# Optimization experiments

Measured on AMD Instinct MI355X. Metric: run time of the kernel, lower is better.

## Reference

```python
import jax, jax.numpy as jnp
import numpy as np

N = 50000        # nodes
E = 800000       # edges (avg degree 16)
OBS = 128        # observation_dim
HID = 64         # hidden_dim (per head)
H1 = 4           # heads in conv1
ACT = 32         # action_dim
NEG_SLOPE = 0.2  # GATv2 default negative_slope


def setup_inputs() -> dict:
    key = jax.random.key(0)
    ks = jax.random.split(key, 10)
    s = 0.05
    x = jax.random.normal(ks[0], (N, OBS), jnp.float32)
    edge_index = jax.random.randint(ks[1], (2, E), 0, N, dtype=jnp.int32)
    # conv1: GATv2Conv(OBS -> HID, heads=4, concat=True)
    W1l = jax.random.normal(ks[2], (OBS, H1 * HID), jnp.float32) * s  # lin_l (source)
    W1r = jax.random.normal(ks[3], (OBS, H1 * HID), jnp.float32) * s  # lin_r (target)
    att1 = jax.random.normal(ks[4], (H1, HID), jnp.float32) * s
    b1 = jnp.zeros((H1 * HID,), jnp.float32)
    # conv2: GATv2Conv(H1*HID -> ACT, heads=1, concat=False)
    W2l = jax.random.normal(ks[5], (H1 * HID, ACT), jnp.float32) * s
    W2r = jax.random.normal(ks[6], (H1 * HID, ACT), jnp.float32) * s
    att2 = jax.random.normal(ks[7], (1, ACT), jnp.float32) * s
    b2 = jnp.zeros((ACT,), jnp.float32)
    return {"x": x, "edge_index": edge_index, "W1l": W1l, "W1r": W1r,
            "att1": att1, "b1": b1, "W2l": W2l, "W2r": W2r,
            "att2": att2, "b2": b2}


def gatv2_layer(x, Wl, Wr, att, bias, src, dst, heads, out_ch, concat):
    """PyG GATv2Conv (add_self_loops=False, share_weights=False)."""
    n = x.shape[0]
    xl = (x @ Wl).reshape(n, heads, out_ch)  # source transform
    xr = (x @ Wr).reshape(n, heads, out_ch)  # target transform
    e = xl[src] + xr[dst]                    # [E, H, C] gathered messages
    g = jnp.where(e > 0, e, NEG_SLOPE * e)   # LeakyReLU
    logits = jnp.einsum('ehc,hc->eh', g, att)  # [E, H]
    # segment softmax over incoming edges of each destination node
    m = jax.ops.segment_max(logits, dst, num_segments=n)      # [N, H]
    ex = jnp.exp(logits - m[dst])
    denom = jax.ops.segment_sum(ex, dst, num_segments=n)      # [N, H]
    alpha = ex / denom[dst]                                   # [E, H]
    out = jax.ops.segment_sum(xl[src] * alpha[:, :, None], dst, num_segments=n)
    out = out.reshape(n, heads * out_ch) if concat else out.mean(axis=1)
    return out + bias


def reference(x, edge_index, W1l, W1r, att1, b1, W2l, W2r, att2, b2):
    src, dst = edge_index[0], edge_index[1]
    h = jax.nn.relu(gatv2_layer(x, W1l, W1r, att1, b1, src, dst, H1, HID, True))
    out = gatv2_layer(h, W2l, W2r, att2, b2, src, dst, 1, ACT, False)
    return out
```

## Files before the change

kernel.cpp:

```cpp
#include <hip/hip_runtime.h>
#include <hip/hip_bf16.h>
#include <math.h>


#define OBS 128
#define HID 64
#define H1 4
#define C1 256
#define ACT 32
#define PAD 128
#define NEG_SLOPE 0.2f
#define LOG2E 1.4426950408889634f

typedef __attribute__((ext_vector_type(2))) _Float16 h2;
typedef __attribute__((ext_vector_type(8))) _Float16 half8;
typedef __attribute__((ext_vector_type(4))) float f32x4;

__device__ inline h2 bc_h2(unsigned u) { return __builtin_bit_cast(h2, u); }
__device__ inline unsigned bc_u(h2 v) { return __builtin_bit_cast(unsigned, v); }
__device__ inline h2 lrelu2(h2 e) {
  const h2 k = {(_Float16)NEG_SLOPE, (_Float16)NEG_SLOPE};
  return __builtin_elementwise_max(e, e * k);
}

__global__ void prep(const float* __restrict__ W1l, const float* __restrict__ W1r,
                     const float* __restrict__ W2l, const float* __restrict__ W2r,
                     _Float16* __restrict__ W1t, _Float16* __restrict__ W2t,
                     const int* __restrict__ src, const int* __restrict__ dst,
                     int* __restrict__ cursor, int* __restrict__ esrc_p,
                     int E, int csrBlocks) {
  int b = blockIdx.x;
  if (b < csrBlocks) {
    int e = b * 256 + threadIdx.x;
    if (e < E) {
      int d = dst[e];
      int slot = atomicAdd(&cursor[d], 1);
      if (slot < PAD) esrc_p[((size_t)d << 7) + slot] = src[e];
    }
    return;
  }
  int i = (b - csrBlocks) * 256 + threadIdx.x;
  if (i < 512 * 128) {
    int n = i >> 7, k = i & 127;
    float v = (n < C1) ? W1l[k * C1 + n] : W1r[k * C1 + (n - C1)];
    W1t[i] = (_Float16)v;
  }
  int j = i - 512 * 128;
  if (j >= 0 && j < 64 * 256) {
    int n = j >> 8, c = j & 255;
    float v = (n < ACT) ? W2l[c * ACT + n] : W2r[c * ACT + (n - ACT)];
    W2t[j] = (_Float16)v;
  }
}

__global__ __launch_bounds__(256) void gemm_mfma1(
    const float* __restrict__ xf,
    const _Float16* __restrict__ W1t,
    _Float16* __restrict__ XLh,
    _Float16* __restrict__ XRh,
    int M) {
  const int LDK = 136;
  __shared__ _Float16 As[128 * 136];
  __shared__ _Float16 Bs[128 * 136];
  const int tid = threadIdx.x;
  const int lane = tid & 63;
  const int wid = tid >> 6;
  const int wm = (wid & 1) * 64, wn = (wid >> 1) * 64;
  const int rowBase = blockIdx.x * 128;
  const int l15 = lane & 15, lq = lane >> 4;

#pragma unroll
  for (int cc = 0; cc < 8; ++cc) {
    int q = cc * 256 + tid;
    int r = q >> 4;
    int kc = (q & 15) * 8;
    int grow = rowBase + r;
    float4 f0 = make_float4(0.f, 0.f, 0.f, 0.f), f1 = f0;
    if (grow < M) {
      f0 = *(const float4*)(xf + (size_t)grow * 128 + kc);
      f1 = *(const float4*)(xf + (size_t)grow * 128 + kc + 4);
    }
    h2 p0 = {(_Float16)f0.x, (_Float16)f0.y};
    h2 p1 = {(_Float16)f0.z, (_Float16)f0.w};
    h2 p2 = {(_Float16)f1.x, (_Float16)f1.y};
    h2 p3 = {(_Float16)f1.z, (_Float16)f1.w};
    *(int4*)(As + r * LDK + kc) = make_int4(bc_u(p0), bc_u(p1), bc_u(p2), bc_u(p3));
  }
#pragma unroll
  for (int cc = 0; cc < 8; ++cc) {
    int q = cc * 256 + tid;
    int r = q >> 4;
    int kc = (q & 15) * 8;
    *(int4*)(Bs + r * LDK + kc) = *(const int4*)(W1t + (size_t)r * 128 + kc);
  }
  __syncthreads();

  for (int cb = 0; cb < 4; ++cb) {
    f32x4 acc[4][4];
#pragma unroll
    for (int i = 0; i < 4; ++i)
#pragma unroll
      for (int j = 0; j < 4; ++j) acc[i][j] = (f32x4){0.f, 0.f, 0.f, 0.f};

#pragma unroll
    for (int ks = 0; ks < 4; ++ks) {
      half8 af[4], bf[4];
#pragma unroll
      for (int t = 0; t < 4; ++t) {
        af[t] = *(const half8*)(As + (wm + t * 16 + l15) * LDK + ks * 32 + lq * 8);
        bf[t] = *(const half8*)(Bs + (wn + t * 16 + l15) * LDK + ks * 32 + lq * 8);
      }
#pragma unroll
      for (int mt = 0; mt < 4; ++mt)
#pragma unroll
        for (int nt = 0; nt < 4; ++nt)
          acc[mt][nt] = __builtin_amdgcn_mfma_f32_16x16x32_f16(
              af[mt], bf[nt], acc[mt][nt], 0, 0, 0);
    }

    _Float16* outp = (cb < 2) ? XLh : XRh;
    int colBase = (cb & 1) * 128;
#pragma unroll
    for (int mt = 0; mt < 4; ++mt) {
#pragma unroll
      for (int r = 0; r < 4; ++r) {
        int row = rowBase + wm + mt * 16 + lq * 4 + r;
        if (row >= M) continue;
#pragma unroll
        for (int nt = 0; nt < 4; ++nt) {
          int col = colBase + wn + nt * 16 + l15;
          outp[(size_t)row * C1 + col] = (_Float16)acc[mt][nt][r];
        }
      }
    }

    if (cb < 3) {
      __syncthreads();
#pragma unroll
      for (int cc = 0; cc < 8; ++cc) {
        int q = cc * 256 + tid;
        int r = q >> 4;
        int kc = (q & 15) * 8;
        *(int4*)(Bs + r * LDK + kc) =
            *(const int4*)(W1t + (size_t)((cb + 1) * 128 + r) * 128 + kc);
      }
      __syncthreads();
    }
  }
}

__global__ __launch_bounds__(256) void gemm_mfma2(
    const _Float16* __restrict__ Hh,
    const _Float16* __restrict__ W2t,
    _Float16* __restrict__ H2h,
    int M) {
  const int LDK = 136;
  __shared__ _Float16 As[128 * 136];
  __shared__ _Float16 Bs[64 * 136];
  const int tid = threadIdx.x;
  const int lane = tid & 63;
  const int wid = tid >> 6;
  const int wm = (wid & 1) * 64, wn = (wid >> 1) * 32;
  const int rowBase = blockIdx.x * 128;

  f32x4 acc[4][2];
#pragma unroll
  for (int i = 0; i < 4; ++i)
#pragma unroll
    for (int j = 0; j < 2; ++j) acc[i][j] = (f32x4){0.f, 0.f, 0.f, 0.f};

  const int l15 = lane & 15, lq = lane >> 4;

  for (int kb = 0; kb < 256; kb += 128) {
#pragma unroll
    for (int cc = 0; cc < 8; ++cc) {
      int q = cc * 256 + tid;
      int r = q >> 4;
      int kc = (q & 15) * 8;
      int grow = rowBase + r;
      int4 av = make_int4(0, 0, 0, 0);
      if (grow < M) av = *(const int4*)(Hh + (size_t)grow * 256 + kb + kc);
      *(int4*)(As + r * LDK + kc) = av;
    }
#pragma unroll
    for (int cc = 0; cc < 4; ++cc) {
      int q = cc * 256 + tid;
      int r = q >> 4;
      int kc = (q & 15) * 8;
      *(int4*)(Bs + r * LDK + kc) = *(const int4*)(W2t + (size_t)r * 256 + kb + kc);
    }
    __syncthreads();

#pragma unroll
    for (int ks = 0; ks < 4; ++ks) {
      half8 af[4], bf[2];
#pragma unroll
      for (int t = 0; t < 4; ++t)
        af[t] = *(const half8*)(As + (wm + t * 16 + l15) * LDK + ks * 32 + lq * 8);
#pragma unroll
      for (int t = 0; t < 2; ++t)
        bf[t] = *(const half8*)(Bs + (wn + t * 16 + l15) * LDK + ks * 32 + lq * 8);
#pragma unroll
      for (int mt = 0; mt < 4; ++mt)
#pragma unroll
        for (int nt = 0; nt < 2; ++nt)
          acc[mt][nt] = __builtin_amdgcn_mfma_f32_16x16x32_f16(
              af[mt], bf[nt], acc[mt][nt], 0, 0, 0);
    }
    __syncthreads();
  }

#pragma unroll
  for (int mt = 0; mt < 4; ++mt) {
#pragma unroll
    for (int r = 0; r < 4; ++r) {
      int row = rowBase + wm + mt * 16 + lq * 4 + r;
      if (row >= M) continue;
#pragma unroll
      for (int nt = 0; nt < 2; ++nt) {
        int col = wn + nt * 16 + l15;
        H2h[(size_t)row * 64 + col] = (_Float16)acc[mt][nt][r];
      }
    }
  }
}

__global__ __launch_bounds__(256) void agg1(const _Float16* __restrict__ XLh,
                                            const _Float16* XRh,
                                            const float* __restrict__ att1,
                                            const float* __restrict__ b1,
                                            const int* __restrict__ degp,
                                            const int* __restrict__ esrc_p,
                                            _Float16* Hh, int n_nodes) {
  int wave = threadIdx.x >> 6;
  int lane = threadIdx.x & 63;
  int n = blockIdx.x * 4 + wave;
  if (n >= n_nodes) return;
  int sl = lane & 31;
  int half = lane >> 5;
  int c8 = sl * 8;

  const char* XLb = (const char*)XLh + c8 * 2;
  int4 xru = *(const int4*)((const char*)XRh + (n << 9) + c8 * 2);
  h2 xr[4] = {bc_h2(xru.x), bc_h2(xru.y), bc_h2(xru.z), bc_h2(xru.w)};
  const float* ap = att1 + (c8 >> 6) * HID + (c8 & 63);
  float4 a0 = *(const float4*)ap;
  float4 a1 = *(const float4*)(ap + 4);
  h2 av[4] = {{(_Float16)(a0.x * LOG2E), (_Float16)(a0.y * LOG2E)},
              {(_Float16)(a0.z * LOG2E), (_Float16)(a0.w * LOG2E)},
              {(_Float16)(a1.x * LOG2E), (_Float16)(a1.y * LOG2E)},
              {(_Float16)(a1.z * LOG2E), (_Float16)(a1.w * LOG2E)}};

  int d = min(degp[n], PAD);
  const int* ep = esrc_p + ((size_t)n << 7);
  float l = 0.f;
  h2 acc[4];
#pragma unroll
  for (int k = 0; k < 4; ++k) acc[k] = (h2){(_Float16)0.f, (_Float16)0.f};

  int base = 0;
  int dmain = d & ~7;
  for (; base < dmain; base += 8) {
    int s0 = ep[base + half];
    int s1 = ep[base + 2 + half];
    int s2 = ep[base + 4 + half];
    int s3 = ep[base + 6 + half];
    int4 u0 = *(const int4*)(XLb + (s0 << 9));
    int4 u1 = *(const int4*)(XLb + (s1 << 9));
    int4 u2 = *(const int4*)(XLb + (s2 << 9));
    int4 u3 = *(const int4*)(XLb + (s3 << 9));
    h2 x0[4] = {bc_h2(u0.x), bc_h2(u0.y), bc_h2(u0.z), bc_h2(u0.w)};
    h2 x1[4] = {bc_h2(u1.x), bc_h2(u1.y), bc_h2(u1.z), bc_h2(u1.w)};
    h2 x2[4] = {bc_h2(u2.x), bc_h2(u2.y), bc_h2(u2.z), bc_h2(u2.w)};
    h2 x3[4] = {bc_h2(u3.x), bc_h2(u3.y), bc_h2(u3.z), bc_h2(u3.w)};
    float c0 = 0.f, c1 = 0.f, c2 = 0.f, c3 = 0.f;
#pragma unroll
    for (int k = 0; k < 4; ++k) {
      c0 = __builtin_amdgcn_fdot2(lrelu2(x0[k] + xr[k]), av[k], c0, false);
      c1 = __builtin_amdgcn_fdot2(lrelu2(x1[k] + xr[k]), av[k], c1, false);
      c2 = __builtin_amdgcn_fdot2(lrelu2(x2[k] + xr[k]), av[k], c2, false);
      c3 = __builtin_amdgcn_fdot2(lrelu2(x3[k] + xr[k]), av[k], c3, false);
    }
    c0 += __shfl_xor(c0, 1); c1 += __shfl_xor(c1, 1);
    c2 += __shfl_xor(c2, 1); c3 += __shfl_xor(c3, 1);
    c0 += __shfl_xor(c0, 2); c1 += __shfl_xor(c1, 2);
    c2 += __shfl_xor(c2, 2); c3 += __shfl_xor(c3, 2);
    c0 += __shfl_xor(c0, 4); c1 += __shfl_xor(c1, 4);
    c2 += __shfl_xor(c2, 4); c3 += __shfl_xor(c3, 4);
    float p0 = __builtin_amdgcn_exp2f(c0);
    float p1 = __builtin_amdgcn_exp2f(c1);
    float p2 = __builtin_amdgcn_exp2f(c2);
    float p3 = __builtin_amdgcn_exp2f(c3);
    l += (p0 + p1) + (p2 + p3);
    _Float16 q0 = (_Float16)p0, q1 = (_Float16)p1, q2 = (_Float16)p2, q3 = (_Float16)p3;
    h2 w0 = {q0, q0}, w1 = {q1, q1}, w2 = {q2, q2}, w3 = {q3, q3};
#pragma unroll
    for (int k = 0; k < 4; ++k)
      acc[k] = acc[k] + w0 * x0[k] + w1 * x1[k] + w2 * x2[k] + w3 * x3[k];
  }
  if (base + 4 <= d) {
    int s0 = ep[base + half];
    int s1 = ep[base + 2 + half];
    int4 u0 = *(const int4*)(XLb + (s0 << 9));
    int4 u1 = *(const int4*)(XLb + (s1 << 9));
    h2 x0[4] = {bc_h2(u0.x), bc_h2(u0.y), bc_h2(u0.z), bc_h2(u0.w)};
    h2 x1[4] = {bc_h2(u1.x), bc_h2(u1.y), bc_h2(u1.z), bc_h2(u1.w)};
    float c0 = 0.f, c1 = 0.f;
#pragma unroll
    for (int k = 0; k < 4; ++k) {
      c0 = __builtin_amdgcn_fdot2(lrelu2(x0[k] + xr[k]), av[k], c0, false);
      c1 = __builtin_amdgcn_fdot2(lrelu2(x1[k] + xr[k]), av[k], c1, false);
    }
    c0 += __shfl_xor(c0, 1); c1 += __shfl_xor(c1, 1);
    c0 += __shfl_xor(c0, 2); c1 += __shfl_xor(c1, 2);
    c0 += __shfl_xor(c0, 4); c1 += __shfl_xor(c1, 4);
    float p0 = __builtin_amdgcn_exp2f(c0);
    float p1 = __builtin_amdgcn_exp2f(c1);
    l += p0 + p1;
    _Float16 q0 = (_Float16)p0, q1 = (_Float16)p1;
    h2 w0 = {q0, q0}, w1 = {q1, q1};
#pragma unroll
    for (int k = 0; k < 4; ++k) acc[k] = acc[k] + w0 * x0[k] + w1 * x1[k];
    base += 4;
  }
  if (base < d) {
    int e0 = base + half, e1 = base + 2 + half;
    bool v0 = e0 < d, v1 = e1 < d;
    int s0 = ep[v0 ? e0 : 0];
    int s1 = ep[v1 ? e1 : 0];
    int4 u0 = *(const int4*)(XLb + (s0 << 9));
    int4 u1 = *(const int4*)(XLb + (s1 << 9));
    h2 x0[4] = {bc_h2(u0.x), bc_h2(u0.y), bc_h2(u0.z), bc_h2(u0.w)};
    h2 x1[4] = {bc_h2(u1.x), bc_h2(u1.y), bc_h2(u1.z), bc_h2(u1.w)};
    float c0 = 0.f, c1 = 0.f;
#pragma unroll
    for (int k = 0; k < 4; ++k) {
      c0 = __builtin_amdgcn_fdot2(lrelu2(x0[k] + xr[k]), av[k], c0, false);
      c1 = __builtin_amdgcn_fdot2(lrelu2(x1[k] + xr[k]), av[k], c1, false);
    }
    c0 += __shfl_xor(c0, 1); c1 += __shfl_xor(c1, 1);
    c0 += __shfl_xor(c0, 2); c1 += __shfl_xor(c1, 2);
    c0 += __shfl_xor(c0, 4); c1 += __shfl_xor(c1, 4);
    float p0 = v0 ? __builtin_amdgcn_exp2f(c0) : 0.f;
    float p1 = v1 ? __builtin_amdgcn_exp2f(c1) : 0.f;
    l += p0 + p1;
    _Float16 q0 = (_Float16)p0, q1 = (_Float16)p1;
    h2 w0 = {q0, q0}, w1 = {q1, q1};
#pragma unroll
    for (int k = 0; k < 4; ++k) acc[k] = acc[k] + w0 * x0[k] + w1 * x1[k];
  }

  l += __shfl_xor(l, 32);
#pragma unroll
  for (int k = 0; k < 4; ++k) {
    unsigned o = __shfl_xor((int)bc_u(acc[k]), 32);
    acc[k] = acc[k] + bc_h2(o);
  }

  float inv = (d > 0) ? 1.f / l : 0.f;
  if (half == 0) {
    float4 b0 = *(const float4*)(b1 + c8);
    float4 b3 = *(const float4*)(b1 + c8 + 4);
    float o0 = fmaxf((float)acc[0][0] * inv + b0.x, 0.f);
    float o1 = fmaxf((float)acc[0][1] * inv + b0.y, 0.f);
    float o2 = fmaxf((float)acc[1][0] * inv + b0.z, 0.f);
    float o3 = fmaxf((float)acc[1][1] * inv + b0.w, 0.f);
    float o4 = fmaxf((float)acc[2][0] * inv + b3.x, 0.f);
    float o5 = fmaxf((float)acc[2][1] * inv + b3.y, 0.f);
    float o6 = fmaxf((float)acc[3][0] * inv + b3.z, 0.f);
    float o7 = fmaxf((float)acc[3][1] * inv + b3.w, 0.f);
    h2 q0 = {(_Float16)o0, (_Float16)o1};
    h2 q1 = {(_Float16)o2, (_Float16)o3};
    h2 q2 = {(_Float16)o4, (_Float16)o5};
    h2 q3 = {(_Float16)o6, (_Float16)o7};
    *(int4*)((char*)Hh + (n << 9) + c8 * 2) =
        make_int4(bc_u(q0), bc_u(q1), bc_u(q2), bc_u(q3));
  }
}

__global__ __launch_bounds__(256) void agg2(const _Float16* __restrict__ H2h,
                                            const float* __restrict__ att2,
                                            const float* __restrict__ b2,
                                            const int* __restrict__ degp,
                                            const int* __restrict__ esrc_p,
                                            float* __restrict__ out, int n_nodes) {
  int wave = threadIdx.x >> 6;
  int lane = threadIdx.x & 63;
  int n = blockIdx.x * 4 + wave;
  if (n >= n_nodes) return;
  int g = lane >> 3;
  int j = lane & 7;
  int c4 = j * 4;

  const char* Hb = (const char*)H2h + c4 * 2;
  uint2 hru = *(const uint2*)((const char*)H2h + (n << 7) + 64 + c4 * 2);
  h2 hr0 = bc_h2(hru.x), hr1 = bc_h2(hru.y);
  float4 af = *(const float4*)(att2 + c4);
  h2 a0 = {(_Float16)(af.x * LOG2E), (_Float16)(af.y * LOG2E)};
  h2 a1 = {(_Float16)(af.z * LOG2E), (_Float16)(af.w * LOG2E)};

  int d = min(degp[n], PAD);
  const int* ep = esrc_p + ((size_t)n << 7);
  float l = 0.f;
  h2 acc0 = {(_Float16)0.f, (_Float16)0.f}, acc1 = acc0;

  int base = 0;
  int dmain = d & ~7;
  for (; base < dmain; base += 8) {
    int s = ep[base + g];
    uint2 u = *(const uint2*)(Hb + (s << 7));
    h2 h0 = bc_h2(u.x), h1 = bc_h2(u.y);
    float c = __builtin_amdgcn_fdot2(lrelu2(h0 + hr0), a0,
              __builtin_amdgcn_fdot2(lrelu2(h1 + hr1), a1, 0.f, false), false);
    c += __shfl_xor(c, 1);
    c += __shfl_xor(c, 2);
    c += __shfl_xor(c, 4);
    float p = __builtin_amdgcn_exp2f(c);
    l += p;
    _Float16 ph = (_Float16)p;
    h2 p2 = {ph, ph};
    acc0 = acc0 + p2 * h0;
    acc1 = acc1 + p2 * h1;
  }
  if (base < d) {
    int e = base + g;
    bool v = e < d;
    int s = ep[v ? e : 0];
    uint2 u = *(const uint2*)(Hb + (s << 7));
    h2 h0 = bc_h2(u.x), h1 = bc_h2(u.y);
    float c = __builtin_amdgcn_fdot2(lrelu2(h0 + hr0), a0,
              __builtin_amdgcn_fdot2(lrelu2(h1 + hr1), a1, 0.f, false), false);
    c += __shfl_xor(c, 1);
    c += __shfl_xor(c, 2);
    c += __shfl_xor(c, 4);
    float p = v ? __builtin_amdgcn_exp2f(c) : 0.f;
    l += p;
    _Float16 ph = (_Float16)p;
    h2 p2 = {ph, ph};
    acc0 = acc0 + p2 * h0;
    acc1 = acc1 + p2 * h1;
  }

#pragma unroll
  for (int o = 8; o < 64; o <<= 1) {
    l += __shfl_xor(l, o);
    acc0 = acc0 + bc_h2((unsigned)__shfl_xor((int)bc_u(acc0), o));
    acc1 = acc1 + bc_h2((unsigned)__shfl_xor((int)bc_u(acc1), o));
  }

  float inv = (d > 0) ? 1.f / l : 0.f;
  if (g == 0) {
    float4 bb = *(const float4*)(b2 + c4);
    float4 o;
    o.x = (float)acc0[0] * inv + bb.x;
    o.y = (float)acc0[1] * inv + bb.y;
    o.z = (float)acc1[0] * inv + bb.z;
    o.w = (float)acc1[1] * inv + bb.w;
    *(float4*)(out + (size_t)n * ACT + c4) = o;
  }
}

extern "C" void kernel_launch(void* const* d_in, const int* in_sizes, int n_in,
                              void* d_out, int out_size, void* d_ws, size_t ws_size,
                              hipStream_t stream) {
  (void)n_in; (void)out_size; (void)ws_size;
  const float* x    = (const float*)d_in[0];
  const int*   ei   = (const int*)d_in[1];
  const float* W1l  = (const float*)d_in[2];
  const float* W1r  = (const float*)d_in[3];
  const float* att1 = (const float*)d_in[4];
  const float* b1   = (const float*)d_in[5];
  const float* W2l  = (const float*)d_in[6];
  const float* W2r  = (const float*)d_in[7];
  const float* att2 = (const float*)d_in[8];
  const float* b2   = (const float*)d_in[9];
  float* out = (float*)d_out;

  const int N = in_sizes[0] / OBS;
  const int E = in_sizes[1] / 2;
  const int* src = ei;
  const int* dst = ei + E;

  _Float16* XLh = (_Float16*)d_ws;
  _Float16* XRh = XLh + (size_t)N * C1;
  _Float16* W1t = XRh + (size_t)N * C1;
  _Float16* W2t = W1t + 512 * 128;
  int* cursor   = (int*)(W2t + 64 * 256);
  int* esrc_p   = cursor + N;
  _Float16* Hh  = XRh;
  _Float16* H2h = XLh;

  (void)hipMemsetAsync(cursor, 0, sizeof(int) * (size_t)N, stream);

  dim3 b256(256);
  int csrBlocks = (E + 255) / 256;
  int packBlocks = (512 * 128 + 64 * 256 + 255) / 256;
  int gr128 = (N + 127) / 128;

  prep<<<csrBlocks + packBlocks, b256, 0, stream>>>(
      W1l, W1r, W2l, W2r, W1t, W2t, src, dst, cursor, esrc_p, E, csrBlocks);
  gemm_mfma1<<<gr128, b256, 0, stream>>>(x, W1t, XLh, XRh, N);
  agg1<<<(N + 3) / 4, b256, 0, stream>>>(XLh, XRh, att1, b1, cursor, esrc_p, Hh, N);
  gemm_mfma2<<<gr128, b256, 0, stream>>>(Hh, W2t, H2h, N);
  agg2<<<(N + 3) / 4, b256, 0, stream>>>(H2h, att2, b2, cursor, esrc_p, out, N);
}
```

Before: 246.4 us.

## Fuse CSR build into GEMM1, shrink edge indices to u16, split agg1 by head

Cursor zeroing moves into the weight-pack kernel, which removes the memset, and the CSR scatter now runs as extra blocks of the first GEMM launch so the two overlap. Source indices in the padded adjacency are stored as 16-bit values, halving index traffic. That only holds while N stays below 65536. agg1 now gives each head its own grid-y slice, with 8 lanes covering one head's 64 channels and 8 edges processed per step. This raises parallelism but re-reads degree and index data once per head. The CSR blocks inherit the GEMM kernel's large shared-memory footprint, which may limit their occupancy.

```diff
diff --git a/kernel.cpp b/kernel.cpp
--- a/kernel.cpp
+++ b/kernel.cpp
@@ -23,23 +23,12 @@
   return __builtin_elementwise_max(e, e * k);
 }
 
-__global__ void prep(const float* __restrict__ W1l, const float* __restrict__ W1r,
-                     const float* __restrict__ W2l, const float* __restrict__ W2r,
-                     _Float16* __restrict__ W1t, _Float16* __restrict__ W2t,
-                     const int* __restrict__ src, const int* __restrict__ dst,
-                     int* __restrict__ cursor, int* __restrict__ esrc_p,
-                     int E, int csrBlocks) {
-  int b = blockIdx.x;
-  if (b < csrBlocks) {
-    int e = b * 256 + threadIdx.x;
-    if (e < E) {
-      int d = dst[e];
-      int slot = atomicAdd(&cursor[d], 1);
-      if (slot < PAD) esrc_p[((size_t)d << 7) + slot] = src[e];
-    }
-    return;
-  }
-  int i = (b - csrBlocks) * 256 + threadIdx.x;
+__global__ void prep0(const float* __restrict__ W1l, const float* __restrict__ W1r,
+                      const float* __restrict__ W2l, const float* __restrict__ W2r,
+                      _Float16* __restrict__ W1t, _Float16* __restrict__ W2t,
+                      int* __restrict__ cursor, int N) {
+  int i = blockIdx.x * 256 + threadIdx.x;
+  if (i < N) cursor[i] = 0;
   if (i < 512 * 128) {
     int n = i >> 7, k = i & 127;
     float v = (n < C1) ? W1l[k * C1 + n] : W1r[k * C1 + (n - C1)];
@@ -53,15 +42,29 @@
   }
 }
 
-__global__ __launch_bounds__(256) void gemm_mfma1(
+__global__ __launch_bounds__(256) void gemm1_csr(
     const float* __restrict__ xf,
     const _Float16* __restrict__ W1t,
     _Float16* __restrict__ XLh,
     _Float16* __restrict__ XRh,
-    int M) {
+    int M,
+    const int* __restrict__ src, const int* __restrict__ dst,
+    int* __restrict__ cursor, unsigned short* __restrict__ esrc_p,
+    int E, int gemmBlocks) {
   const int LDK = 136;
   __shared__ _Float16 As[128 * 136];
   __shared__ _Float16 Bs[128 * 136];
+
+  if ((int)blockIdx.x >= gemmBlocks) {
+    int e = ((int)blockIdx.x - gemmBlocks) * 256 + threadIdx.x;
+    if (e < E) {
+      int d = dst[e];
+      int slot = atomicAdd(&cursor[d], 1);
+      if (slot < PAD) esrc_p[((size_t)d << 7) + slot] = (unsigned short)src[e];
+    }
+    return;
+  }
+
   const int tid = threadIdx.x;
   const int lane = tid & 63;
   const int wid = tid >> 6;
@@ -230,20 +233,21 @@
                                             const float* __restrict__ att1,
                                             const float* __restrict__ b1,
                                             const int* __restrict__ degp,
-                                            const int* __restrict__ esrc_p,
+                                            const unsigned short* __restrict__ esrc_p,
                                             _Float16* Hh, int n_nodes) {
   int wave = threadIdx.x >> 6;
   int lane = threadIdx.x & 63;
   int n = blockIdx.x * 4 + wave;
+  int head = blockIdx.y;
   if (n >= n_nodes) return;
-  int sl = lane & 31;
-  int half = lane >> 5;
-  int c8 = sl * 8;
-
-  const char* XLb = (const char*)XLh + c8 * 2;
-  int4 xru = *(const int4*)((const char*)XRh + (n << 9) + c8 * 2);
+  int g = lane >> 3;
+  int j = lane & 7;
+  int co = head * 128 + j * 16;
+
+  const char* XLb = (const char*)XLh + co;
+  int4 xru = *(const int4*)((const char*)XRh + ((size_t)n << 9) + co);
   h2 xr[4] = {bc_h2(xru.x), bc_h2(xru.y), bc_h2(xru.z), bc_h2(xru.w)};
-  const float* ap = att1 + (c8 >> 6) * HID + (c8 & 63);
+  const float* ap = att1 + head * HID + j * 8;
   float4 a0 = *(const float4*)ap;
   float4 a1 = *(const float4*)(ap + 4);
   h2 av[4] = {{(_Float16)(a0.x * LOG2E), (_Float16)(a0.y * LOG2E)},
@@ -252,57 +256,19 @@
               {(_Float16)(a1.z * LOG2E), (_Float16)(a1.w * LOG2E)}};
 
   int d = min(degp[n], PAD);
-  const int* ep = esrc_p + ((size_t)n << 7);
+  const unsigned short* ep = esrc_p + ((size_t)n << 7);
   float l = 0.f;
   h2 acc[4];
 #pragma unroll
   for (int k = 0; k < 4; ++k) acc[k] = (h2){(_Float16)0.f, (_Float16)0.f};
 
   int base = 0;
-  int dmain = d & ~7;
-  for (; base < dmain; base += 8) {
-    int s0 = ep[base + half];
-    int s1 = ep[base + 2 + half];
-    int s2 = ep[base + 4 + half];
-    int s3 = ep[base + 6 + half];
-    int4 u0 = *(const int4*)(XLb + (s0 << 9));
-    int4 u1 = *(const int4*)(XLb + (s1 << 9));
-    int4 u2 = *(const int4*)(XLb + (s2 << 9));
-    int4 u3 = *(const int4*)(XLb + (s3 << 9));
-    h2 x0[4] = {bc_h2(u0.x), bc_h2(u0.y), bc_h2(u0.z), bc_h2(u0.w)};
-    h2 x1[4] = {bc_h2(u1.x), bc_h2(u1.y), bc_h2(u1.z), bc_h2(u1.w)};
-    h2 x2[4] = {bc_h2(u2.x), bc_h2(u2.y), bc_h2(u2.z), bc_h2(u2.w)};
-    h2 x3[4] = {bc_h2(u3.x), bc_h2(u3.y), bc_h2(u3.z), bc_h2(u3.w)};
-    float c0 = 0.f, c1 = 0.f, c2 = 0.f, c3 = 0.f;
-#pragma unroll
-    for (int k = 0; k < 4; ++k) {
-      c0 = __builtin_amdgcn_fdot2(lrelu2(x0[k] + xr[k]), av[k], c0, false);
-      c1 = __builtin_amdgcn_fdot2(lrelu2(x1[k] + xr[k]), av[k], c1, false);
-      c2 = __builtin_amdgcn_fdot2(lrelu2(x2[k] + xr[k]), av[k], c2, false);
-      c3 = __builtin_amdgcn_fdot2(lrelu2(x3[k] + xr[k]), av[k], c3, false);
-    }
-    c0 += __shfl_xor(c0, 1); c1 += __shfl_xor(c1, 1);
-    c2 += __shfl_xor(c2, 1); c3 += __shfl_xor(c3, 1);
-    c0 += __shfl_xor(c0, 2); c1 += __shfl_xor(c1, 2);
-    c2 += __shfl_xor(c2, 2); c3 += __shfl_xor(c3, 2);
-    c0 += __shfl_xor(c0, 4); c1 += __shfl_xor(c1, 4);
-    c2 += __shfl_xor(c2, 4); c3 += __shfl_xor(c3, 4);
-    float p0 = __builtin_amdgcn_exp2f(c0);
-    float p1 = __builtin_amdgcn_exp2f(c1);
-    float p2 = __builtin_amdgcn_exp2f(c2);
-    float p3 = __builtin_amdgcn_exp2f(c3);
-    l += (p0 + p1) + (p2 + p3);
-    _Float16 q0 = (_Float16)p0, q1 = (_Float16)p1, q2 = (_Float16)p2, q3 = (_Float16)p3;
-    h2 w0 = {q0, q0}, w1 = {q1, q1}, w2 = {q2, q2}, w3 = {q3, q3};
-#pragma unroll
-    for (int k = 0; k < 4; ++k)
-      acc[k] = acc[k] + w0 * x0[k] + w1 * x1[k] + w2 * x2[k] + w3 * x3[k];
-  }
-  if (base + 4 <= d) {
-    int s0 = ep[base + half];
-    int s1 = ep[base + 2 + half];
-    int4 u0 = *(const int4*)(XLb + (s0 << 9));
-    int4 u1 = *(const int4*)(XLb + (s1 << 9));
+  int dmain = d & ~15;
+  for (; base < dmain; base += 16) {
+    int s0 = ep[base + g];
+    int s1 = ep[base + 8 + g];
+    int4 u0 = *(const int4*)(XLb + ((size_t)s0 << 9));
+    int4 u1 = *(const int4*)(XLb + ((size_t)s1 << 9));
     h2 x0[4] = {bc_h2(u0.x), bc_h2(u0.y), bc_h2(u0.z), bc_h2(u0.w)};
     h2 x1[4] = {bc_h2(u1.x), bc_h2(u1.y), bc_h2(u1.z), bc_h2(u1.w)};
     float c0 = 0.f, c1 = 0.f;
@@ -321,46 +287,60 @@
     h2 w0 = {q0, q0}, w1 = {q1, q1};
 #pragma unroll
     for (int k = 0; k < 4; ++k) acc[k] = acc[k] + w0 * x0[k] + w1 * x1[k];
-    base += 4;
+  }
+  if (base + 8 <= d) {
+    int s0 = ep[base + g];
+    int4 u0 = *(const int4*)(XLb + ((size_t)s0 << 9));
+    h2 x0[4] = {bc_h2(u0.x), bc_h2(u0.y), bc_h2(u0.z), bc_h2(u0.w)};
+    float c0 = 0.f;
+#pragma unroll
+    for (int k = 0; k < 4; ++k)
+      c0 = __builtin_amdgcn_fdot2(lrelu2(x0[k] + xr[k]), av[k], c0, false);
+    c0 += __shfl_xor(c0, 1);
+    c0 += __shfl_xor(c0, 2);
+    c0 += __shfl_xor(c0, 4);
+    float p0 = __builtin_amdgcn_exp2f(c0);
+    l += p0;
+    _Float16 q0 = (_Float16)p0;
+    h2 w0 = {q0, q0};
+#pragma unroll
+    for (int k = 0; k < 4; ++k) acc[k] = acc[k] + w0 * x0[k];
+    base += 8;
   }
   if (base < d) {
-    int e0 = base + half, e1 = base + 2 + half;
-    bool v0 = e0 < d, v1 = e1 < d;
-    int s0 = ep[v0 ? e0 : 0];
-    int s1 = ep[v1 ? e1 : 0];
-    int4 u0 = *(const int4*)(XLb + (s0 << 9));
-    int4 u1 = *(const int4*)(XLb + (s1 << 9));
+    int e = base + g;
+    bool v = e < d;
+    int s0 = ep[v ? e : 0];
+    int4 u0 = *(const int4*)(XLb + ((size_t)s0 << 9));
     h2 x0[4] = {bc_h2(u0.x), bc_h2(u0.y), bc_h2(u0.z), bc_h2(u0.w)};
-    h2 x1[4] = {bc_h2(u1.x), bc_h2(u1.y), bc_h2(u1.z), bc_h2(u1.w)};
-    float c0 = 0.f, c1 = 0.f;
-#pragma unroll
-    for (int k = 0; k < 4; ++k) {
+    float c0 = 0.f;
+#pragma unroll
+    for (int k = 0; k < 4; ++k)
       c0 = __builtin_amdgcn_fdot2(lrelu2(x0[k] + xr[k]), av[k], c0, false);
-      c1 = __builtin_amdgcn_fdot2(lrelu2(x1[k] + xr[k]), av[k], c1, false);
-    }
-    c0 += __shfl_xor(c0, 1); c1 += __shfl_xor(c1, 1);
-    c0 += __shfl_xor(c0, 2); c1 += __shfl_xor(c1, 2);
-    c0 += __shfl_xor(c0, 4); c1 += __shfl_xor(c1, 4);
-    float p0 = v0 ? __builtin_amdgcn_exp2f(c0) : 0.f;
-    float p1 = v1 ? __builtin_amdgcn_exp2f(c1) : 0.f;
-    l += p0 + p1;
-    _Float16 q0 = (_Float16)p0, q1 = (_Float16)p1;
-    h2 w0 = {q0, q0}, w1 = {q1, q1};
-#pragma unroll
-    for (int k = 0; k < 4; ++k) acc[k] = acc[k] + w0 * x0[k] + w1 * x1[k];
-  }
-
-  l += __shfl_xor(l, 32);
-#pragma unroll
-  for (int k = 0; k < 4; ++k) {
-    unsigned o = __shfl_xor((int)bc_u(acc[k]), 32);
-    acc[k] = acc[k] + bc_h2(o);
+    c0 += __shfl_xor(c0, 1);
+    c0 += __shfl_xor(c0, 2);
+    c0 += __shfl_xor(c0, 4);
+    float p0 = v ? __builtin_amdgcn_exp2f(c0) : 0.f;
+    l += p0;
+    _Float16 q0 = (_Float16)p0;
+    h2 w0 = {q0, q0};
+#pragma unroll
+    for (int k = 0; k < 4; ++k) acc[k] = acc[k] + w0 * x0[k];
+  }
+
+#pragma unroll
+  for (int o = 8; o < 64; o <<= 1) {
+    l += __shfl_xor(l, o);
+#pragma unroll
+    for (int k = 0; k < 4; ++k)
+      acc[k] = acc[k] + bc_h2((unsigned)__shfl_xor((int)bc_u(acc[k]), o));
   }
 
   float inv = (d > 0) ? 1.f / l : 0.f;
-  if (half == 0) {
-    float4 b0 = *(const float4*)(b1 + c8);
-    float4 b3 = *(const float4*)(b1 + c8 + 4);
+  if (g == 0) {
+    const float* bp = b1 + head * HID + j * 8;
+    float4 b0 = *(const float4*)bp;
+    float4 b3 = *(const float4*)(bp + 4);
     float o0 = fmaxf((float)acc[0][0] * inv + b0.x, 0.f);
     float o1 = fmaxf((float)acc[0][1] * inv + b0.y, 0.f);
     float o2 = fmaxf((float)acc[1][0] * inv + b0.z, 0.f);
@@ -373,7 +353,7 @@
     h2 q1 = {(_Float16)o2, (_Float16)o3};
     h2 q2 = {(_Float16)o4, (_Float16)o5};
     h2 q3 = {(_Float16)o6, (_Float16)o7};
-    *(int4*)((char*)Hh + (n << 9) + c8 * 2) =
+    *(int4*)((char*)Hh + ((size_t)n << 9) + co) =
         make_int4(bc_u(q0), bc_u(q1), bc_u(q2), bc_u(q3));
   }
 }
@@ -382,7 +362,7 @@
                                             const float* __restrict__ att2,
                                             const float* __restrict__ b2,
                                             const int* __restrict__ degp,
-                                            const int* __restrict__ esrc_p,
+                                            const unsigned short* __restrict__ esrc_p,
                                             float* __restrict__ out, int n_nodes) {
   int wave = threadIdx.x >> 6;
   int lane = threadIdx.x & 63;
@@ -393,14 +373,14 @@
   int c4 = j * 4;
 
   const char* Hb = (const char*)H2h + c4 * 2;
-  uint2 hru = *(const uint2*)((const char*)H2h + (n << 7) + 64 + c4 * 2);
+  uint2 hru = *(const uint2*)((const char*)H2h + ((size_t)n << 7) + 64 + c4 * 2);
   h2 hr0 = bc_h2(hru.x), hr1 = bc_h2(hru.y);
   float4 af = *(const float4*)(att2 + c4);
   h2 a0 = {(_Float16)(af.x * LOG2E), (_Float16)(af.y * LOG2E)};
   h2 a1 = {(_Float16)(af.z * LOG2E), (_Float16)(af.w * LOG2E)};
 
   int d = min(degp[n], PAD);
-  const int* ep = esrc_p + ((size_t)n << 7);
+  const unsigned short* ep = esrc_p + ((size_t)n << 7);
   float l = 0.f;
   h2 acc0 = {(_Float16)0.f, (_Float16)0.f}, acc1 = acc0;
 
@@ -408,7 +388,7 @@
   int dmain = d & ~7;
   for (; base < dmain; base += 8) {
     int s = ep[base + g];
-    uint2 u = *(const uint2*)(Hb + (s << 7));
+    uint2 u = *(const uint2*)(Hb + ((size_t)s << 7));
     h2 h0 = bc_h2(u.x), h1 = bc_h2(u.y);
     float c = __builtin_amdgcn_fdot2(lrelu2(h0 + hr0), a0,
               __builtin_amdgcn_fdot2(lrelu2(h1 + hr1), a1, 0.f, false), false);
@@ -426,7 +406,7 @@
     int e = base + g;
     bool v = e < d;
     int s = ep[v ? e : 0];
-    uint2 u = *(const uint2*)(Hb + (s << 7));
+    uint2 u = *(const uint2*)(Hb + ((size_t)s << 7));
     h2 h0 = bc_h2(u.x), h1 = bc_h2(u.y);
     float c = __builtin_amdgcn_fdot2(lrelu2(h0 + hr0), a0,
               __builtin_amdgcn_fdot2(lrelu2(h1 + hr1), a1, 0.f, false), false);
@@ -486,21 +466,20 @@
   _Float16* W1t = XRh + (size_t)N * C1;
   _Float16* W2t = W1t + 512 * 128;
   int* cursor   = (int*)(W2t + 64 * 256);
-  int* esrc_p   = cursor + N;
+  unsigned short* esrc_p = (unsigned short*)(cursor + N);
   _Float16* Hh  = XRh;
   _Float16* H2h = XLh;
 
-  (void)hipMemsetAsync(cursor, 0, sizeof(int) * (size_t)N, stream);
-
   dim3 b256(256);
   int csrBlocks = (E + 255) / 256;
-  int packBlocks = (512 * 128 + 64 * 256 + 255) / 256;
-  int gr128 = (N + 127) / 128;
-
-  prep<<<csrBlocks + packBlocks, b256, 0, stream>>>(
-      W1l, W1r, W2l, W2r, W1t, W2t, src, dst, cursor, esrc_p, E, csrBlocks);
-  gemm_mfma1<<<gr128, b256, 0, stream>>>(x, W1t, XLh, XRh, N);
-  agg1<<<(N + 3) / 4, b256, 0, stream>>>(XLh, XRh, att1, b1, cursor, esrc_p, Hh, N);
-  gemm_mfma2<<<gr128, b256, 0, stream>>>(Hh, W2t, H2h, N);
+  int gemmBlocks = (N + 127) / 128;
+  int prepBlocks = (512 * 128 + 64 * 256 + 255) / 256;
+
+  prep0<<<prepBlocks, b256, 0, stream>>>(W1l, W1r, W2l, W2r, W1t, W2t, cursor, N);
+  gemm1_csr<<<gemmBlocks + csrBlocks, b256, 0, stream>>>(
+      x, W1t, XLh, XRh, N, src, dst, cursor, esrc_p, E, gemmBlocks);
+  agg1<<<dim3((N + 3) / 4, 4), b256, 0, stream>>>(
+      XLh, XRh, att1, b1, cursor, esrc_p, Hh, N);
+  gemm_mfma2<<<gemmBlocks, b256, 0, stream>>>(Hh, W2t, H2h, N);
   agg2<<<(N + 3) / 4, b256, 0, stream>>>(H2h, att2, b2, cursor, esrc_p, out, N);
 }
```

Result: slower. 276.3 us (+12.1%).
